# Kernel tuning notes

Measured on AMD Instinct MI355X. Metric: run time of the kernel, lower is better.

## Reference

```python
import jax, jax.numpy as jnp
import numpy as np

B, N, DIM, H = 2, 4096, 512, 8
DH = DIM // H  # head dim = 64


def setup_inputs() -> dict:
    key = jax.random.key(0)
    kx, kw, kb = jax.random.split(key, 3)
    x = jax.random.normal(kx, (B, N, DIM), dtype=jnp.float32)
    W = jax.random.normal(kw, (DIM, 3 * DIM), dtype=jnp.float32) / np.sqrt(DIM)
    b = jax.random.normal(kb, (3 * DIM,), dtype=jnp.float32) * 0.02
    return {"x": x, "W": W, "b": b}


def reference(x, W, b):
    Bx, n, d = x.shape
    qvk = x @ W + b  # [B, n, 3*dim]
    # torch.chunk order in source: q, v, k
    q, v, k = jnp.split(qvk, 3, axis=-1)

    def heads(t):  # [B, n, dim] -> [B, h, n, dh]
        return t.reshape(Bx, n, H, DH).transpose(0, 2, 1, 3)

    q, v, k = heads(q), heads(v), heads(k)
    # full (non-fused) attention: materializes [B, h, n, n] scores
    scale = jnp.einsum('bhqd,bhkd->bhqk', q, k) / jnp.sqrt(jnp.float32(DH))
    atn = jax.nn.softmax(scale, axis=-1)
    out = jnp.einsum('bhqk,bhkd->bhqd', atn, v)  # [B, h, n, dh]
    # concat_head: [B, h, n, dh] -> [B, n, h*dh]
    out = out.transpose(0, 2, 1, 3).reshape(Bx, n, H * DH)
    return out
```

## Files before the change

### kernel.cpp

```cpp
#include <hip/hip_runtime.h>
#include <hip/hip_bf16.h>
#include <math.h>

#define BB    2
#define NN    4096
#define DIM   512
#define NH    8
#define DH    64
#define NC    1536
#define MM    (BB*NN)

typedef __bf16 bf16x8 __attribute__((ext_vector_type(8)));
typedef __bf16 bf16x4 __attribute__((ext_vector_type(4)));
typedef float  f32x4  __attribute__((ext_vector_type(4)));

#define QSCALE 0.18033688011112042f

__device__ __forceinline__ int swz(int c) { return c ^ (((c >> 3) ^ (c >> 6)) & 7); }

__device__ __forceinline__ void gl_lds16(const __hip_bfloat16* g, __bf16* l) {
    __builtin_amdgcn_global_load_lds(
        (const __attribute__((address_space(1))) unsigned int*)g,
        (__attribute__((address_space(3))) unsigned int*)l, 16, 0, 0);
}

__device__ __forceinline__ int sniff(const unsigned short* x) {
    unsigned short v = x[2 * (threadIdx.x & 63)];
    int e = (v >> 7) & 0xFF;
    unsigned long long m = __ballot(e >= 110 && e <= 140);
    return __popcll(m) >= 48;
}

__global__ __launch_bounds__(256) void prep_kernel(
    const void* __restrict__ xin, const void* __restrict__ win,
    const void* __restrict__ bin,
    __hip_bfloat16* __restrict__ Xb, __hip_bfloat16* __restrict__ WT,
    float* __restrict__ Bf)
{
    __shared__ __bf16 tile[64][68];
    int bfmode = sniff((const unsigned short*)xin);
    int bid = blockIdx.x;
    int t = threadIdx.x;
    if (bid < 2048) {
        if (bfmode) return;
        int i = (bid * 256 + t) * 8;
        const float* xf = (const float*)xin + i;
        bf16x8 v;
        for (int j = 0; j < 8; j++) v[j] = (__bf16)xf[j];
        *(bf16x8*)(Xb + i) = v;
    } else if (bid < 2048 + 192) {
        int tl = bid - 2048;
        int kt = tl / 24, nt = tl % 24;
        int tx = t & 63, tyq = t >> 6;
        for (int r = 0; r < 16; r++) {
            int kl = r * 4 + tyq;
            int gi = (kt * 64 + kl) * NC + nt * 64 + tx;
            float v = bfmode ? __bfloat162float(((const __hip_bfloat16*)win)[gi])
                             : ((const float*)win)[gi];
            tile[kl][tx] = (__bf16)v;
        }
        __syncthreads();
        for (int r = 0; r < 16; r++) {
            int nl = r * 4 + tyq;
            WT[(size_t)(nt * 64 + nl) * DIM + kt * 64 + tx] = (__hip_bfloat16)(float)tile[tx][nl];
        }
    } else {
        int i = (bid - 2048 - 192) * 256 + t;
        if (i < NC)
            Bf[i] = bfmode ? __bfloat162float(((const __hip_bfloat16*)bin)[i])
                           : ((const float*)bin)[i];
    }
}

__global__ __launch_bounds__(256, 3) void qkv_gemm(
    const unsigned short* __restrict__ xs,
    const __hip_bfloat16* __restrict__ Xb,
    const __hip_bfloat16* __restrict__ WT,
    const float* __restrict__ Bf,
    __hip_bfloat16* __restrict__ Qb,
    __hip_bfloat16* __restrict__ Kb,
    __hip_bfloat16* __restrict__ Vt)
{
    __shared__ __align__(16) __bf16 smem[16384];
    __bf16* Xs = smem;
    __bf16* Ws = smem + 8192;

    int bfmode = sniff(xs);
    const __hip_bfloat16* X = bfmode ? (const __hip_bfloat16*)xs : Xb;

    int wave = threadIdx.x >> 6, lane = threadIdx.x & 63;
    int lane16 = lane & 15, quad = lane >> 4;
    int bm = blockIdx.x / 12, bn = blockIdx.x % 12;
    int m0b = bm * 128, n0b = bn * 128;
    int wm = wave >> 1, wn = wave & 1;
    int m0 = m0b + wm * 64, n0 = n0b + wn * 64;

    int xgo[2], sbase[2];
    for (int j = 0; j < 2; j++) {
        int p = (wave * 2 + j) * 64 + lane;
        int g = swz(p);
        xgo[j] = (g >> 2) * DIM + (g & 3) * 8;
        sbase[j] = (wave * 2 + j) * 512;
    }
    int aoff[4], boff[4];
    for (int mi = 0; mi < 4; mi++)
        aoff[mi] = swz((wm * 64 + mi * 16 + lane16) * 4 + quad) * 8;
    for (int ni = 0; ni < 4; ni++)
        boff[ni] = swz((wn * 64 + ni * 16 + lane16) * 4 + quad) * 8;

    const __hip_bfloat16* Xg = X  + (size_t)m0b * DIM;
    const __hip_bfloat16* Wg = WT + (size_t)n0b * DIM;

    for (int j = 0; j < 2; j++) {
        gl_lds16(Xg + xgo[j], &Xs[sbase[j]]);
        gl_lds16(Wg + xgo[j], &Ws[sbase[j]]);
    }
    __syncthreads();

    f32x4 acc[4][4] = {};
    for (int k0 = 0; k0 < DIM; k0 += 32) {
        int cur = (k0 >> 5) & 1, nbuf = cur ^ 1;
        int k1 = (k0 + 32) & (DIM - 1);
        for (int j = 0; j < 2; j++) {
            gl_lds16(Xg + k1 + xgo[j], &Xs[nbuf * 4096 + sbase[j]]);
            gl_lds16(Wg + k1 + xgo[j], &Ws[nbuf * 4096 + sbase[j]]);
        }
        bf16x8 a[4], b[4];
        for (int mi = 0; mi < 4; mi++) a[mi] = *(const bf16x8*)&Xs[cur * 4096 + aoff[mi]];
        for (int ni = 0; ni < 4; ni++) b[ni] = *(const bf16x8*)&Ws[cur * 4096 + boff[ni]];
        for (int mi = 0; mi < 4; mi++)
            for (int ni = 0; ni < 4; ni++)
                acc[mi][ni] = __builtin_amdgcn_mfma_f32_16x16x32_bf16(a[mi], b[ni], acc[mi][ni], 0, 0, 0);
        __syncthreads();
    }
    __bf16* epi = smem + wave * 4096;

    int sec = n0b >> 9;
    int bidx = m0b >> 12;
    if (sec == 1) {
        for (int ni = 0; ni < 4; ni++) {
            int nloc = ni * 16 + lane16;
            float bv = Bf[n0 + nloc];
            for (int mi = 0; mi < 4; mi++) {
                bf16x4 pk;
                for (int r = 0; r < 4; r++) pk[r] = (__bf16)(acc[mi][ni][r] + bv);
                int idx = swz(nloc * 8 + mi * 2 + (quad >> 1)) * 8 + (quad & 1) * 4;
                *(bf16x4*)&epi[idx] = pk;
            }
        }
        int hl = (n0 - 512) >> 6;
        int mbase = m0b - bidx * NN + wm * 64;
        for (int p = 0; p < 8; p++) {
            int n = p * 8 + (lane >> 3), mc = lane & 7;
            bf16x8 vv = *(const bf16x8*)&epi[swz(n * 8 + mc) * 8];
            *(bf16x8*)(Vt + ((size_t)(bidx * 8 + hl) * 64 + n) * NN + mbase + mc * 8) = vv;
        }
    } else {
        bool isQ = (sec == 0);
        int h = (n0 & 511) >> 6;
        for (int mi = 0; mi < 4; mi++) {
            for (int ni = 0; ni < 4; ni++) {
                float bv = Bf[n0 + ni * 16 + lane16];
                int dl = ni * 16 + lane16;
                for (int r = 0; r < 4; r++) {
                    int row = mi * 16 + quad * 4 + r;
                    float v = acc[mi][ni][r] + bv;
                    if (isQ) v *= QSCALE;
                    epi[swz(row * 8 + (dl >> 3)) * 8 + (dl & 7)] = (__bf16)v;
                }
            }
        }
        __hip_bfloat16* dst = isQ ? Qb : Kb;
        int bh = bidx * 8 + h;
        int mbase = m0 - bidx * NN;
        for (int p = 0; p < 8; p++) {
            int row = p * 8 + (lane >> 3), dc = lane & 7;
            bf16x8 vv = *(const bf16x8*)&epi[swz(row * 8 + dc) * 8];
            *(bf16x8*)(dst + ((size_t)bh * NN + mbase + row) * DH + dc * 8) = vv;
        }
    }
}

__global__ __launch_bounds__(128, 2) void attn_kernel(
    const __hip_bfloat16* __restrict__ Qb,
    const __hip_bfloat16* __restrict__ Kb,
    const __hip_bfloat16* __restrict__ Vt,
    void* __restrict__ OutV,
    const unsigned short* __restrict__ xs)
{
    __shared__ __align__(16) __bf16 Kst[2][4096];
    __shared__ __align__(16) __bf16 Vst[2][4096];
    __shared__ __align__(16) __bf16 Pp[2][2048];

    int bfmode = sniff(xs);
    int wave = threadIdx.x >> 6, lane = threadIdx.x & 63;
    int lane16 = lane & 15, quad = lane >> 4;
    int i = blockIdx.x;
    int bh = i & 15;
    int qt = i >> 4;
    int q0 = qt * 64 + wave * 32;

    const __hip_bfloat16* Qh = Qb + (size_t)bh * NN * DH;
    const __hip_bfloat16* Kh = Kb + (size_t)bh * NN * DH;
    const __hip_bfloat16* Vh = Vt + (size_t)bh * DH * NN;

    bf16x8 aq[2][2];
    for (int rf = 0; rf < 2; rf++)
        for (int kc = 0; kc < 2; kc++)
            aq[rf][kc] = *(const bf16x8*)(Qh + (size_t)(q0 + rf * 16 + lane16) * DH + kc * 32 + quad * 8);

    int kgo[4], vgo[4], sbase[4];
    for (int j = 0; j < 4; j++) {
        int p = (wave * 4 + j) * 64 + lane;
        int g = swz(p);
        kgo[j] = (g >> 3) * DH + (g & 7) * 8;
        vgo[j] = (g >> 3) * NN + (g & 7) * 8;
        sbase[j] = (wave * 4 + j) * 512;
    }
    int koff[4][2], voff[4][2], poffr[2][2], poffw[2][4];
    for (int kf = 0; kf < 4; kf++)
        for (int kc = 0; kc < 2; kc++)
            koff[kf][kc] = swz((4 * lane16 + kf) * 8 + kc * 4 + quad) * 8;
    for (int dt = 0; dt < 4; dt++)
        for (int kc = 0; kc < 2; kc++)
            voff[dt][kc] = swz((dt * 16 + lane16) * 8 + kc * 4 + quad) * 8;
    for (int rf = 0; rf < 2; rf++) {
        for (int kc = 0; kc < 2; kc++)
            poffr[rf][kc] = swz((rf * 16 + lane16) * 8 + kc * 4 + quad) * 8;
        for (int r = 0; r < 4; r++)
            poffw[rf][r] = swz((rf * 16 + quad * 4 + r) * 8 + (lane16 >> 1)) * 8 + (lane16 & 1) * 4;
    }

    for (int j = 0; j < 4; j++) {
        gl_lds16(Kh + kgo[j], &Kst[0][sbase[j]]);
        gl_lds16(Vh + vgo[j], &Vst[0][sbase[j]]);
    }
    __syncthreads();

    bf16x8 vones;
    for (int j = 0; j < 8; j++) vones[j] = (__bf16)1.0f;
    f32x4 o[2][4] = {};
    f32x4 ol[2] = {};

    for (int k0 = 0; k0 < NN; k0 += 64) {
        int cur = (k0 >> 6) & 1, nb = cur ^ 1;
        int k1 = (k0 + 64) & (NN - 1);
        for (int j = 0; j < 4; j++) {
            gl_lds16(Kh + (size_t)k1 * DH + kgo[j], &Kst[nb][sbase[j]]);
            gl_lds16(Vh + k1 + vgo[j], &Vst[nb][sbase[j]]);
        }

        bf16x8 kb[4][2], vb[4][2];
        for (int kf = 0; kf < 4; kf++)
            for (int kc = 0; kc < 2; kc++)
                kb[kf][kc] = *(const bf16x8*)&Kst[cur][koff[kf][kc]];
        for (int dt = 0; dt < 4; dt++)
            for (int kc = 0; kc < 2; kc++)
                vb[dt][kc] = *(const bf16x8*)&Vst[cur][voff[dt][kc]];

        f32x4 s[2][4];
        for (int rf = 0; rf < 2; rf++)
            for (int kf = 0; kf < 4; kf++) {
                f32x4 t = {};
                t = __builtin_amdgcn_mfma_f32_16x16x32_bf16(aq[rf][0], kb[kf][0], t, 0, 0, 0);
                t = __builtin_amdgcn_mfma_f32_16x16x32_bf16(aq[rf][1], kb[kf][1], t, 0, 0, 0);
                s[rf][kf] = t;
            }

        for (int rf = 0; rf < 2; rf++)
            for (int r = 0; r < 4; r++) {
                bf16x4 pk;
                pk[0] = (__bf16)__builtin_amdgcn_exp2f(fminf(s[rf][0][r], 60.0f));
                pk[1] = (__bf16)__builtin_amdgcn_exp2f(fminf(s[rf][1][r], 60.0f));
                pk[2] = (__bf16)__builtin_amdgcn_exp2f(fminf(s[rf][2][r], 60.0f));
                pk[3] = (__bf16)__builtin_amdgcn_exp2f(fminf(s[rf][3][r], 60.0f));
                *(bf16x4*)&Pp[wave][poffw[rf][r]] = pk;
            }
        bf16x8 pa[2][2];
        for (int rf = 0; rf < 2; rf++)
            for (int kc = 0; kc < 2; kc++)
                pa[rf][kc] = *(const bf16x8*)&Pp[wave][poffr[rf][kc]];

        for (int rf = 0; rf < 2; rf++) {
            for (int dt = 0; dt < 4; dt++) {
                o[rf][dt] = __builtin_amdgcn_mfma_f32_16x16x32_bf16(pa[rf][0], vb[dt][0], o[rf][dt], 0, 0, 0);
                o[rf][dt] = __builtin_amdgcn_mfma_f32_16x16x32_bf16(pa[rf][1], vb[dt][1], o[rf][dt], 0, 0, 0);
            }
            ol[rf] = __builtin_amdgcn_mfma_f32_16x16x32_bf16(pa[rf][0], vones, ol[rf], 0, 0, 0);
            ol[rf] = __builtin_amdgcn_mfma_f32_16x16x32_bf16(pa[rf][1], vones, ol[rf], 0, 0, 0);
        }

        __syncthreads();
    }

    for (int rf = 0; rf < 2; rf++) {
        float rinv[4];
        for (int r = 0; r < 4; r++) rinv[r] = 1.0f / ol[rf][r];
        for (int dt = 0; dt < 4; dt++)
            for (int r = 0; r < 4; r++) {
                int row = rf * 16 + quad * 4 + r;
                int d = dt * 16 + lane16;
                Pp[wave][swz(row * 8 + (d >> 3)) * 8 + (d & 7)] = (__bf16)(o[rf][dt][r] * rinv[r]);
            }
    }
    int bidx = bh >> 3, h = bh & 7;
    for (int p = 0; p < 4; p++) {
        int row = p * 8 + (lane >> 3), mc = lane & 7;
        bf16x8 vv = *(const bf16x8*)&Pp[wave][swz(row * 8 + mc) * 8];
        size_t base = ((size_t)bidx * NN + q0 + row) * DIM + h * 64 + mc * 8;
        if (bfmode) {
            *(bf16x8*)((__hip_bfloat16*)OutV + base) = vv;
        } else {
            float* op = (float*)OutV + base;
            f32x4 f0, f1;
            for (int j = 0; j < 4; j++) { f0[j] = (float)vv[j]; f1[j] = (float)vv[4 + j]; }
            *(f32x4*)op = f0;
            *(f32x4*)(op + 4) = f1;
        }
    }
}

extern "C" void kernel_launch(void* const* d_in, const int* in_sizes, int n_in,
                              void* d_out, int out_size, void* d_ws, size_t ws_size,
                              hipStream_t stream) {
    char* ws = (char*)d_ws;
    __hip_bfloat16* WT = (__hip_bfloat16*)ws;
    __hip_bfloat16* Xb = WT + (size_t)NC * DIM;
    float* Bf = (float*)(Xb + (size_t)MM * DIM);
    __hip_bfloat16* Qb = (__hip_bfloat16*)(Bf + NC);
    __hip_bfloat16* Kb = Qb + (size_t)BB * NH * NN * DH;
    __hip_bfloat16* Vt = Kb + (size_t)BB * NH * NN * DH;

    prep_kernel<<<2048 + 192 + 6, 256, 0, stream>>>(d_in[0], d_in[1], d_in[2], Xb, WT, Bf);
    qkv_gemm<<<(MM / 128) * (NC / 128), 256, 0, stream>>>(
        (const unsigned short*)d_in[0], Xb, WT, Bf, Qb, Kb, Vt);
    attn_kernel<<<1024, 128, 0, stream>>>(Qb, Kb, Vt, d_out, (const unsigned short*)d_in[0]);
}
```

Measured before the change: 199.1 us.

## Compute transposed scores so P feeds PV MFMA from registers without LDS

Swaps MFMA operand roles so the score tile is computed as S^T (keys by queries). The exp'd probabilities then sit in registers in the B-operand layout of the 16x16x16 bf16 MFMA and feed the PV product directly, with no LDS round trip. V fragments are read as 4-element slices with new offsets, and the output epilogue reuses K staging memory. This also skips the wasted wrap-around prefetch on the last iteration. It uses twice as many smaller PV MFMAs and more LDS reads of V, plus a fallback path when the builtin is absent.

Measured after the change: 209.2 us. 5.1% more time.

```diff
diff --git a/kernel.cpp b/kernel.cpp
--- a/kernel.cpp
+++ b/kernel.cpp
@@ -13,8 +13,15 @@
 typedef __bf16 bf16x8 __attribute__((ext_vector_type(8)));
 typedef __bf16 bf16x4 __attribute__((ext_vector_type(4)));
 typedef float  f32x4  __attribute__((ext_vector_type(4)));
+typedef short  s16x4  __attribute__((ext_vector_type(4)));
 
 #define QSCALE 0.18033688011112042f
+
+#if __has_builtin(__builtin_amdgcn_mfma_f32_16x16x16bf16_1k)
+#define HAVE_M16 1
+#else
+#define HAVE_M16 0
+#endif
 
 __device__ __forceinline__ int swz(int c) { return c ^ (((c >> 3) ^ (c >> 6)) & 7); }
 
@@ -30,6 +37,16 @@
     unsigned long long m = __ballot(e >= 110 && e <= 140);
     return __popcll(m) >= 48;
 }
+
+__device__ __forceinline__ f32x4 mfma32(bf16x8 a, bf16x8 b, f32x4 c) {
+    return __builtin_amdgcn_mfma_f32_16x16x32_bf16(a, b, c, 0, 0, 0);
+}
+#if HAVE_M16
+__device__ __forceinline__ f32x4 pv16(bf16x4 a, bf16x4 b, f32x4 c) {
+    return __builtin_amdgcn_mfma_f32_16x16x16bf16_1k(
+        __builtin_bit_cast(s16x4, a), __builtin_bit_cast(s16x4, b), c, 0, 0, 0);
+}
+#endif
 
 __global__ __launch_bounds__(256) void prep_kernel(
     const void* __restrict__ xin, const void* __restrict__ win,
@@ -130,7 +147,7 @@
         for (int ni = 0; ni < 4; ni++) b[ni] = *(const bf16x8*)&Ws[cur * 4096 + boff[ni]];
         for (int mi = 0; mi < 4; mi++)
             for (int ni = 0; ni < 4; ni++)
-                acc[mi][ni] = __builtin_amdgcn_mfma_f32_16x16x32_bf16(a[mi], b[ni], acc[mi][ni], 0, 0, 0);
+                acc[mi][ni] = mfma32(a[mi], b[ni], acc[mi][ni]);
         __syncthreads();
     }
     __bf16* epi = smem + wave * 4096;
@@ -190,7 +207,9 @@
 {
     __shared__ __align__(16) __bf16 Kst[2][4096];
     __shared__ __align__(16) __bf16 Vst[2][4096];
-    __shared__ __align__(16) __bf16 Pp[2][2048];
+#if !HAVE_M16
+    __shared__ __align__(16) __bf16 Pq[2][2560];
+#endif
 
     int bfmode = sniff(xs);
     int wave = threadIdx.x >> 6, lane = threadIdx.x & 63;
@@ -204,10 +223,10 @@
     const __hip_bfloat16* Kh = Kb + (size_t)bh * NN * DH;
     const __hip_bfloat16* Vh = Vt + (size_t)bh * DH * NN;
 
-    bf16x8 aq[2][2];
-    for (int rf = 0; rf < 2; rf++)
+    bf16x8 bq[2][2];
+    for (int qf = 0; qf < 2; qf++)
         for (int kc = 0; kc < 2; kc++)
-            aq[rf][kc] = *(const bf16x8*)(Qh + (size_t)(q0 + rf * 16 + lane16) * DH + kc * 32 + quad * 8);
+            bq[qf][kc] = *(const bf16x8*)(Qh + (size_t)(q0 + qf * 16 + lane16) * DH + kc * 32 + quad * 8);
 
     int kgo[4], vgo[4], sbase[4];
     for (int j = 0; j < 4; j++) {
@@ -217,19 +236,21 @@
         vgo[j] = (g >> 3) * NN + (g & 7) * 8;
         sbase[j] = (wave * 4 + j) * 512;
     }
-    int koff[4][2], voff[4][2], poffr[2][2], poffw[2][4];
+    int koff[4][2];
     for (int kf = 0; kf < 4; kf++)
         for (int kc = 0; kc < 2; kc++)
-            koff[kf][kc] = swz((4 * lane16 + kf) * 8 + kc * 4 + quad) * 8;
+            koff[kf][kc] = swz((kf * 16 + lane16) * 8 + kc * 4 + quad) * 8;
+#if HAVE_M16
+    int voff[4][4];
     for (int dt = 0; dt < 4; dt++)
-        for (int kc = 0; kc < 2; kc++)
-            voff[dt][kc] = swz((dt * 16 + lane16) * 8 + kc * 4 + quad) * 8;
-    for (int rf = 0; rf < 2; rf++) {
-        for (int kc = 0; kc < 2; kc++)
-            poffr[rf][kc] = swz((rf * 16 + lane16) * 8 + kc * 4 + quad) * 8;
-        for (int r = 0; r < 4; r++)
-            poffw[rf][r] = swz((rf * 16 + quad * 4 + r) * 8 + (lane16 >> 1)) * 8 + (lane16 & 1) * 4;
-    }
+        for (int kf = 0; kf < 4; kf++)
+            voff[dt][kf] = swz((dt * 16 + lane16) * 8 + kf * 2 + (quad >> 1)) * 8 + (quad & 1) * 4;
+#else
+    int voff[4][2];
+    for (int dt = 0; dt < 4; dt++)
+        for (int kh = 0; kh < 2; kh++)
+            voff[dt][kh] = swz((dt * 16 + lane16) * 8 + kh * 4 + quad) * 8;
+#endif
 
     for (int j = 0; j < 4; j++) {
         gl_lds16(Kh + kgo[j], &Kst[0][sbase[j]]);
@@ -237,76 +258,87 @@
     }
     __syncthreads();
 
-    bf16x8 vones;
-    for (int j = 0; j < 8; j++) vones[j] = (__bf16)1.0f;
-    f32x4 o[2][4] = {};
+    f32x4 o[4][2] = {};
     f32x4 ol[2] = {};
+#if HAVE_M16
+    bf16x4 onesA;
+    for (int j = 0; j < 4; j++) onesA[j] = (__bf16)1.0f;
+#else
+    bf16x8 onesA8;
+    for (int j = 0; j < 8; j++) onesA8[j] = (__bf16)1.0f;
+#endif
 
     for (int k0 = 0; k0 < NN; k0 += 64) {
         int cur = (k0 >> 6) & 1, nb = cur ^ 1;
-        int k1 = (k0 + 64) & (NN - 1);
-        for (int j = 0; j < 4; j++) {
-            gl_lds16(Kh + (size_t)k1 * DH + kgo[j], &Kst[nb][sbase[j]]);
-            gl_lds16(Vh + k1 + vgo[j], &Vst[nb][sbase[j]]);
-        }
-
-        bf16x8 kb[4][2], vb[4][2];
+        if (k0 + 64 < NN) {
+            int k1 = k0 + 64;
+            for (int j = 0; j < 4; j++) {
+                gl_lds16(Kh + (size_t)k1 * DH + kgo[j], &Kst[nb][sbase[j]]);
+                gl_lds16(Vh + k1 + vgo[j], &Vst[nb][sbase[j]]);
+            }
+        }
+
+        bf16x8 ka[4][2];
         for (int kf = 0; kf < 4; kf++)
             for (int kc = 0; kc < 2; kc++)
-                kb[kf][kc] = *(const bf16x8*)&Kst[cur][koff[kf][kc]];
-        for (int dt = 0; dt < 4; dt++)
-            for (int kc = 0; kc < 2; kc++)
-                vb[dt][kc] = *(const bf16x8*)&Vst[cur][voff[dt][kc]];
-
-        f32x4 s[2][4];
-        for (int rf = 0; rf < 2; rf++)
-            for (int kf = 0; kf < 4; kf++) {
+                ka[kf][kc] = *(const bf16x8*)&Kst[cur][koff[kf][kc]];
+        f32x4 s[4][2];
+        for (int kf = 0; kf < 4; kf++)
+            for (int qf = 0; qf < 2; qf++) {
                 f32x4 t = {};
-                t = __builtin_amdgcn_mfma_f32_16x16x32_bf16(aq[rf][0], kb[kf][0], t, 0, 0, 0);
-                t = __builtin_amdgcn_mfma_f32_16x16x32_bf16(aq[rf][1], kb[kf][1], t, 0, 0, 0);
-                s[rf][kf] = t;
-            }
-
-        for (int rf = 0; rf < 2; rf++)
-            for (int r = 0; r < 4; r++) {
-                bf16x4 pk;
-                pk[0] = (__bf16)__builtin_amdgcn_exp2f(fminf(s[rf][0][r], 60.0f));
-                pk[1] = (__bf16)__builtin_amdgcn_exp2f(fminf(s[rf][1][r], 60.0f));
-                pk[2] = (__bf16)__builtin_amdgcn_exp2f(fminf(s[rf][2][r], 60.0f));
-                pk[3] = (__bf16)__builtin_amdgcn_exp2f(fminf(s[rf][3][r], 60.0f));
-                *(bf16x4*)&Pp[wave][poffw[rf][r]] = pk;
-            }
-        bf16x8 pa[2][2];
-        for (int rf = 0; rf < 2; rf++)
-            for (int kc = 0; kc < 2; kc++)
-                pa[rf][kc] = *(const bf16x8*)&Pp[wave][poffr[rf][kc]];
-
-        for (int rf = 0; rf < 2; rf++) {
-            for (int dt = 0; dt < 4; dt++) {
-                o[rf][dt] = __builtin_amdgcn_mfma_f32_16x16x32_bf16(pa[rf][0], vb[dt][0], o[rf][dt], 0, 0, 0);
-                o[rf][dt] = __builtin_amdgcn_mfma_f32_16x16x32_bf16(pa[rf][1], vb[dt][1], o[rf][dt], 0, 0, 0);
-            }
-            ol[rf] = __builtin_amdgcn_mfma_f32_16x16x32_bf16(pa[rf][0], vones, ol[rf], 0, 0, 0);
-            ol[rf] = __builtin_amdgcn_mfma_f32_16x16x32_bf16(pa[rf][1], vones, ol[rf], 0, 0, 0);
-        }
-
+                t = mfma32(ka[kf][0], bq[qf][0], t);
+                t = mfma32(ka[kf][1], bq[qf][1], t);
+                s[kf][qf] = t;
+            }
+
+        bf16x4 pt[4][2];
+        for (int kf = 0; kf < 4; kf++)
+            for (int qf = 0; qf < 2; qf++)
+                for (int r = 0; r < 4; r++)
+                    pt[kf][qf][r] = (__bf16)__builtin_amdgcn_exp2f(fminf(s[kf][qf][r], 60.0f));
+
+#if HAVE_M16
+        for (int kf = 0; kf < 4; kf++) {
+            bf16x4 av[4];
+            for (int dt = 0; dt < 4; dt++) av[dt] = *(const bf16x4*)&Vst[cur][voff[dt][kf]];
+            for (int qf = 0; qf < 2; qf++) {
+                for (int dt = 0; dt < 4; dt++)
+                    o[dt][qf] = pv16(av[dt], pt[kf][qf], o[dt][qf]);
+                ol[qf] = pv16(onesA, pt[kf][qf], ol[qf]);
+            }
+        }
+#else
+        for (int kf = 0; kf < 4; kf++)
+            for (int qf = 0; qf < 2; qf++)
+                for (int r = 0; r < 4; r++)
+                    Pq[wave][(qf * 16 + lane16) * 80 + kf * 16 + quad * 4 + r] = pt[kf][qf][r];
+        for (int qf = 0; qf < 2; qf++)
+            for (int kh = 0; kh < 2; kh++) {
+                bf16x8 pb = *(const bf16x8*)&Pq[wave][(qf * 16 + lane16) * 80 + kh * 32 + quad * 8];
+                for (int dt = 0; dt < 4; dt++) {
+                    bf16x8 av = *(const bf16x8*)&Vst[cur][voff[dt][kh]];
+                    o[dt][qf] = mfma32(av, pb, o[dt][qf]);
+                }
+                ol[qf] = mfma32(onesA8, pb, ol[qf]);
+            }
+#endif
         __syncthreads();
     }
 
-    for (int rf = 0; rf < 2; rf++) {
-        float rinv[4];
-        for (int r = 0; r < 4; r++) rinv[r] = 1.0f / ol[rf][r];
+    __bf16* epi = &Kst[0][0] + wave * 2048;
+    for (int qf = 0; qf < 2; qf++) {
+        float rinv = 1.0f / ol[qf][0];
         for (int dt = 0; dt < 4; dt++)
             for (int r = 0; r < 4; r++) {
-                int row = rf * 16 + quad * 4 + r;
-                int d = dt * 16 + lane16;
-                Pp[wave][swz(row * 8 + (d >> 3)) * 8 + (d & 7)] = (__bf16)(o[rf][dt][r] * rinv[r]);
+                int d = dt * 16 + quad * 4 + r;
+                int row = qf * 16 + lane16;
+                epi[swz(row * 8 + (d >> 3)) * 8 + (d & 7)] = (__bf16)(o[dt][qf][r] * rinv);
             }
     }
     int bidx = bh >> 3, h = bh & 7;
     for (int p = 0; p < 4; p++) {
         int row = p * 8 + (lane >> 3), mc = lane & 7;
-        bf16x8 vv = *(const bf16x8*)&Pp[wave][swz(row * 8 + mc) * 8];
+        bf16x8 vv = *(const bf16x8*)&epi[swz(row * 8 + mc) * 8];
         size_t base = ((size_t)bidx * NN + q0 + row) * DIM + h * 64 + mc * 8;
         if (bfmode) {
             *(bf16x8*)((__hip_bfloat16*)OutV + base) = vv;
```
